# Optimization experiments

Measured on AMD Instinct MI355X. Metric: run time of the kernel, lower is better.

## Reference

```python
import jax, jax.numpy as jnp
import numpy as np

NPOINT = 1024
RADIUS = 0.5
NSAMPLE = 32
BN_EPS = 1e-5


def square_distance(src, dst):
    # src: (B,S,3), dst: (B,N,3) -> (B,S,N)
    return (jnp.sum(src ** 2, -1, keepdims=True)
            + jnp.swapaxes(jnp.sum(dst ** 2, -1, keepdims=True), -2, -1)
            - 2.0 * jnp.einsum('bsc,bnc->bsn', src, dst))


def farthest_point_sample(xyz, npoint):
    # xyz: (B,N,3) -> (B,npoint) int32. Deterministic start at index 0.
    B, N, _ = xyz.shape

    def step(carry, _):
        distance, farthest = carry
        centroid = jnp.take_along_axis(xyz, farthest[:, None, None], axis=1)  # (B,1,3)
        d = jnp.sum((xyz - centroid) ** 2, axis=-1)                           # (B,N)
        distance = jnp.minimum(distance, d)
        nxt = jnp.argmax(distance, axis=-1).astype(jnp.int32)
        return (distance, nxt), farthest

    init = (jnp.full((B, N), 1e10, dtype=xyz.dtype), jnp.zeros((B,), jnp.int32))
    _, cents = jax.lax.scan(step, init, None, length=npoint)  # (npoint,B)
    return cents.T


def ball_query(radius, nsample, xyz, new_xyz):
    # -> (B,S,nsample) int32 indices into N; empty slots padded with first hit.
    B, N, _ = xyz.shape
    dist = square_distance(new_xyz, xyz)                       # (B,S,N)
    base = jnp.arange(N, dtype=jnp.int32)[None, None, :]
    idx = jnp.where(dist <= radius ** 2, base, N)
    idx = jnp.sort(idx, axis=-1)[:, :, :nsample]
    first = idx[:, :, :1]
    return jnp.where(idx == N, first, idx)


def index_points(points, idx):
    # points: (B,N,C), idx: (B,...) -> (B,...,C)
    return jax.vmap(lambda p, i: p[i])(points, idx)


def _forward(xyz, features, params):
    # indices are data-dependent but non-differentiable selections
    xyz_c = jax.lax.stop_gradient(xyz)
    fps_idx = farthest_point_sample(xyz_c, NPOINT)             # (B,S)
    group_idx = ball_query(RADIUS, NSAMPLE, xyz_c, index_points(xyz_c, fps_idx))

    new_xyz = index_points(xyz, fps_idx)                       # (B,S,3)
    grouped_xyz = index_points(xyz, group_idx) - new_xyz[:, :, None, :]  # (B,S,K,3)
    grouped = jnp.concatenate([grouped_xyz, index_points(features, group_idx)], -1)  # (B,S,K,Cin)

    for (w, b, g, be) in params:
        # 1x1 Conv2d == per-point linear; BatchNorm2d in training mode:
        # stats over all but channel axis (here axes 0,1,2 of (B,S,K,C)).
        h = jnp.einsum('bskc,dc->bskd', grouped, w) + b
        mean = jnp.mean(h, axis=(0, 1, 2))
        var = jnp.var(h, axis=(0, 1, 2))
        h = (h - mean) * jax.lax.rsqrt(var + BN_EPS) * g + be
        grouped = jax.nn.gelu(h, approximate=False)

    new_features = jnp.max(grouped, axis=2)                    # (B,S,D)
    return new_xyz, new_features


def setup_inputs() -> dict:
    key = jax.random.key(0)
    ks = jax.random.split(key, 16)
    B, N, C = 16, 4096, 64
    inp = {
        'xyz': jax.random.normal(ks[0], (B, N, 3), jnp.float32),
        'features': jax.random.normal(ks[1], (B, N, C), jnp.float32),
    }
    chans = [67, 64, 64, 128]
    for i in range(3):
        cin, cout = chans[i], chans[i + 1]
        inp[f'w{i}'] = jax.random.normal(ks[2 + 4 * i], (cout, cin), jnp.float32) * (1.0 / np.sqrt(cin))
        inp[f'b{i}'] = jnp.zeros((cout,), jnp.float32)
        inp[f'g{i}'] = jnp.ones((cout,), jnp.float32)
        inp[f'be{i}'] = jnp.zeros((cout,), jnp.float32)
    return inp


def reference(xyz, features, w0, b0, g0, be0, w1, b1, g1, be1, w2, b2, g2, be2):
    params = [(w0, b0, g0, be0), (w1, b1, g1, be1), (w2, b2, g2, be2)]
    return _forward(xyz, features, params)
```

## Files before the change

### kernel.cpp

```cpp
#include <hip/hip_runtime.h>

typedef unsigned int uint;
typedef unsigned short ushort;

#define NB 16
#define NN 4096
#define NS 1024
#define NK 32
#define CIN0 67
#define NPTS (NB*NS*NK)
#define BN_EPS 1e-5f
#define INV_NPTS (1.0f/524288.0f)

#define W0T_OFF 0
#define W1T_OFF 4288
#define W2T_OFF 8384
#define WT_TOTAL 16576

#define FPS_T 256
#define PPT (NN / FPS_T)

__device__ __forceinline__ void amax_merge(float& bv, int& bi, float ov, int oi) {
  if (ov > bv || (ov == bv && oi < bi)) { bv = ov; bi = oi; }
}

#define DPP_AMAX_STEP(CTRL) do { \
    int _ov = __builtin_amdgcn_update_dpp(0, __float_as_int(bv), (CTRL), 0xF, 0xF, true); \
    int _oi = __builtin_amdgcn_update_dpp(0, bi,                 (CTRL), 0xF, 0xF, true); \
    amax_merge(bv, bi, __int_as_float(_ov), _oi); \
  } while (0)

__global__ __launch_bounds__(FPS_T) void fps_kernel(
    const float* __restrict__ xyz, float* __restrict__ centers,
    float* __restrict__ out_newxyz)
{
#pragma clang fp contract(off)
  __shared__ float4 sxyz[NN];
  __shared__ int sfar[NS];
  __shared__ __align__(16) uint2 sred[2][FPS_T/64];
  const int b = blockIdx.x;
  const int tid = threadIdx.x;
  const float* xb = xyz + (size_t)b * NN * 3;
  for (int i = tid; i < NN; i += FPS_T)
    sxyz[i] = make_float4(xb[i*3+0], xb[i*3+1], xb[i*3+2], 0.f);
  __syncthreads();
  float px[PPT], py[PPT], pz[PPT], dist[PPT];
  const int base = tid * PPT;
#pragma unroll
  for (int j = 0; j < PPT; ++j) {
    float4 P = sxyz[base+j];
    px[j] = P.x; py[j] = P.y; pz[j] = P.z;
    dist[j] = 1e10f;
  }
  float4 C0 = sxyz[0];
  float cx = C0.x, cy = C0.y, cz = C0.z;
  if (tid == 0) sfar[0] = 0;

  for (int it = 1; it < NS; ++it) {
#pragma unroll
    for (int j = 0; j < PPT; ++j) {
      float dx = px[j]-cx, dy = py[j]-cy, dz = pz[j]-cz;
      float d = (dx*dx + dy*dy) + dz*dz;
      float dd = dist[j];
      dist[j] = d < dd ? d : dd;
    }
    float v8[8]; int i8[8];
#pragma unroll
    for (int j = 0; j < 8; ++j) {
      bool t = dist[2*j+1] > dist[2*j];
      v8[j] = t ? dist[2*j+1] : dist[2*j];
      i8[j] = base + (t ? 2*j+1 : 2*j);
    }
    float v4[4]; int i4[4];
#pragma unroll
    for (int j = 0; j < 4; ++j) {
      bool t = v8[2*j+1] > v8[2*j];
      v4[j] = t ? v8[2*j+1] : v8[2*j];
      i4[j] = t ? i8[2*j+1] : i8[2*j];
    }
    float v2[2]; int i2[2];
#pragma unroll
    for (int j = 0; j < 2; ++j) {
      bool t = v4[2*j+1] > v4[2*j];
      v2[j] = t ? v4[2*j+1] : v4[2*j];
      i2[j] = t ? i4[2*j+1] : i4[2*j];
    }
    bool t0 = v2[1] > v2[0];
    float bv = t0 ? v2[1] : v2[0];
    int   bi = t0 ? i2[1] : i2[0];
    DPP_AMAX_STEP(0x121);
    DPP_AMAX_STEP(0x122);
    DPP_AMAX_STEP(0x124);
    DPP_AMAX_STEP(0x128);
    DPP_AMAX_STEP(0x142);
    DPP_AMAX_STEP(0x143);
    const int pb = it & 1;
    if ((tid & 63) == 63) sred[pb][tid>>6] = make_uint2(__float_as_uint(bv), (uint)bi);
    __syncthreads();
    uint4 ra = *((const uint4*)&sred[pb][0]);
    uint4 rb = *((const uint4*)&sred[pb][2]);
    float fv = __uint_as_float(ra.x); int fi = (int)ra.y;
    amax_merge(fv, fi, __uint_as_float(ra.z), (int)ra.w);
    amax_merge(fv, fi, __uint_as_float(rb.x), (int)rb.y);
    amax_merge(fv, fi, __uint_as_float(rb.z), (int)rb.w);
    float4 C = sxyz[fi];
    cx = C.x; cy = C.y; cz = C.z;
    if (tid == 0) sfar[it] = fi;
  }
  __syncthreads();
  for (int s = tid; s < NS; s += FPS_T) {
    int f = sfar[s];
    float4 C = sxyz[f];
    size_t o = ((size_t)b * NS + s) * 3;
    centers[o] = C.x; centers[o+1] = C.y; centers[o+2] = C.z;
    out_newxyz[o] = C.x; out_newxyz[o+1] = C.y; out_newxyz[o+2] = C.z;
  }
}

#define BPAD(i) ((i) + ((i)>>6))
__global__ __launch_bounds__(256,2) void ball_kernel(
    const float* __restrict__ xyz, const float* __restrict__ centers,
    int* __restrict__ group_idx)
{
#pragma clang fp contract(off)
  __shared__ float sx[4160], sy[4160], sz[4160], sq[4160];
  const int bid = blockIdx.x;
  const int b = bid >> 6;
  const int c0 = (bid & 63) << 4;
  const int tid = threadIdx.x;
  const int lane = tid & 63;
  const int wave = tid >> 6;
  const float* xb = xyz + (size_t)b * NN * 3;
  for (int i = tid; i < NN; i += 256) {
    float x = xb[i*3+0], y = xb[i*3+1], z = xb[i*3+2];
    int a = BPAD(i);
    sx[a] = x; sy[a] = y; sz[a] = z;
    sq[a] = (x*x + y*y) + z*z;
  }
  __syncthreads();
  const int a0 = lane * 65;
#pragma unroll 1
  for (int r = 0; r < 4; ++r) {
    const int s = c0 + wave*4 + r;
    const size_t co = ((size_t)b * NS + s) * 3;
    const float cx = centers[co], cy = centers[co+1], cz = centers[co+2];
    const float csq = (cx*cx + cy*cy) + cz*cz;
    unsigned long long mask = 0ull;
#pragma unroll 8
    for (int j = 0; j < 64; ++j) {
      const float dot = (cx*sx[a0+j] + cy*sy[a0+j]) + cz*sz[a0+j];
      const float dist = (csq + sq[a0+j]) - 2.0f*dot;
      mask |= ((unsigned long long)(dist <= 0.25f)) << j;
    }
    int cnt = __popcll(mask);
    int inc = cnt;
#pragma unroll
    for (int m = 1; m < 64; m <<= 1) {
      int o = __shfl_up(inc, m);
      if (lane >= m) inc += o;
    }
    const int pre = inc - cnt;
    const int total = __shfl(inc, 63);
    unsigned long long bal = __ballot(cnt > 0);
    int fl = __ffsll(bal) - 1;
    int myfirst = cnt ? (lane << 6) + __ffsll(mask) - 1 : 0;
    int firstG = __shfl(myfirst, fl);
    int* out = group_idx + ((size_t)b * NS + s) * NK;
    if (pre < NK && cnt) {
      int k = pre;
      unsigned long long m2 = mask;
      while (m2 && k < NK) {
        int j = __ffsll(m2) - 1;
        out[k++] = (lane << 6) + j;
        m2 &= m2 - 1;
      }
    }
    if (total < NK) {
      for (int q2 = total + lane; q2 < NK; q2 += 64) out[q2] = firstG;
    }
  }
}

__global__ __launch_bounds__(256) void prep_kernel(
    const float* __restrict__ w0, const float* __restrict__ w1,
    const float* __restrict__ w2, float* __restrict__ wT)
{
  int i = blockIdx.x*256 + threadIdx.x;
  if (i < 4288) {
    int c = i >> 6, d = i & 63;
    wT[i] = w0[d*CIN0 + c];
  } else if (i < 8384) {
    int j = i - 4288; int c = j >> 6, d = j & 63;
    wT[i] = w1[d*64 + c];
  } else if (i < WT_TOTAL) {
    int j = i - 8384; int c = j >> 7, d = j & 127;
    wT[i] = w2[d*64 + c];
  }
}

__device__ __forceinline__ float gelu_f(float x) {
  float z = fabsf(x) * 0.70710678118654752f;
  float t = __builtin_amdgcn_rcpf(fmaf(0.3275911f, z, 1.0f));
  float p = t * fmaf(t, fmaf(t, fmaf(t, fmaf(t, 1.061405429f, -1.453152027f),
                                     1.421413741f), -0.284496736f), 0.254829592f);
  float ex = __expf(-z*z);
  float er = fmaf(-p, ex, 1.0f);
  float se = __uint_as_float(__float_as_uint(er) | (__float_as_uint(x) & 0x80000000u));
  return 0.5f * x * (1.0f + se);
}
__device__ __forceinline__ float bf_lo(uint u) { return __uint_as_float(u << 16); }
__device__ __forceinline__ float bf_hi(uint u) { return __uint_as_float(u & 0xffff0000u); }
__device__ __forceinline__ uint bfpack(float a, float b) {
  uint ua = __float_as_uint(a), ub = __float_as_uint(b);
  ua = (ua + 0x7fffu + ((ua >> 16) & 1u)) >> 16;
  ub = (ub + 0x7fffu + ((ub >> 16) & 1u)) >> 16;
  return (ua & 0xffffu) | (ub << 16);
}

__device__ __forceinline__ void fmac64(float (&acc)[64], const float* wrow, float xc) {
  const float4* wp = (const float4*)wrow;
#pragma unroll
  for (int i = 0; i < 16; ++i) {
    float4 w = wp[i];
    acc[i*4+0] = fmaf(xc, w.x, acc[i*4+0]);
    acc[i*4+1] = fmaf(xc, w.y, acc[i*4+1]);
    acc[i*4+2] = fmaf(xc, w.z, acc[i*4+2]);
    acc[i*4+3] = fmaf(xc, w.w, acc[i*4+3]);
  }
}
__device__ __forceinline__ void fmac128(float (&acc)[128], const float* wrow, float xc) {
  const float4* wp = (const float4*)wrow;
#pragma unroll
  for (int i = 0; i < 32; ++i) {
    float4 w = wp[i];
    acc[i*4+0] = fmaf(xc, w.x, acc[i*4+0]);
    acc[i*4+1] = fmaf(xc, w.y, acc[i*4+1]);
    acc[i*4+2] = fmaf(xc, w.z, acc[i*4+2]);
    acc[i*4+3] = fmaf(xc, w.w, acc[i*4+3]);
  }
}

__device__ __forceinline__ void layer0(
    const float* __restrict__ xyz, const float* __restrict__ feat,
    const float* __restrict__ centers, const int* __restrict__ gidx,
    const float* wsh, const float* b0v, int p, float (&acc)[64])
{
  const int b = p >> 15;
  const int s = (p & 32767) >> 5;
  const int gi = gidx[p];
#pragma unroll
  for (int d = 0; d < 64; ++d) acc[d] = b0v[d];
  const float* cp = centers + ((size_t)(b*NS + s))*3;
  const float* pp = xyz + ((size_t)(b*NN) + gi)*3;
  const float4* fr = (const float4*)(feat + ((size_t)(b*NN) + gi)*64);
  float4 f = fr[0];
  fmac64(acc, wsh + 0*64, pp[0]-cp[0]);
  fmac64(acc, wsh + 1*64, pp[1]-cp[1]);
  fmac64(acc, wsh + 2*64, pp[2]-cp[2]);
#pragma unroll 1
  for (int q = 0; q < 16; ++q) {
    const int nq = (q < 15) ? q + 1 : 15;
    float4 fn = fr[nq];
    fmac64(acc, wsh + (3+q*4)*64, f.x);
    fmac64(acc, wsh + (4+q*4)*64, f.y);
    fmac64(acc, wsh + (5+q*4)*64, f.z);
    fmac64(acc, wsh + (6+q*4)*64, f.w);
    f = fn;
  }
}

__device__ __forceinline__ void block_colsum64(const float (&v)[64], float* sbuf,
    float* bsum, float* bssq, int cbase)
{
  const int tid = threadIdx.x;
#pragma unroll
  for (int cc = 0; cc < 4; ++cc) {
    __syncthreads();
#pragma unroll
    for (int j = 0; j < 16; ++j) sbuf[tid*17 + j] = v[cc*16 + j];
    __syncthreads();
    const int c = tid & 15, seg = tid >> 4;
    float s = 0.f, q = 0.f;
#pragma unroll
    for (int i = 0; i < 16; ++i) {
      float x = sbuf[(seg*16 + i)*17 + c];
      s += x; q += x*x;
    }
    __syncthreads();
    sbuf[tid*2] = s; sbuf[tid*2+1] = q;
    __syncthreads();
    if (tid < 16) {
      float ss = 0.f, qq = 0.f;
#pragma unroll
      for (int sg = 0; sg < 16; ++sg) {
        ss += sbuf[(sg*16 + tid)*2];
        qq += sbuf[(sg*16 + tid)*2 + 1];
      }
      bsum[cbase + cc*16 + tid] += ss;
      bssq[cbase + cc*16 + tid] += qq;
    }
  }
  __syncthreads();
}

__global__ __launch_bounds__(256,3) void p0_kernel(
    const float* __restrict__ xyz, const float* __restrict__ feat,
    const float* __restrict__ centers, const int* __restrict__ gidx,
    const float* __restrict__ wT, const float* __restrict__ b0,
    ushort* __restrict__ X, float* __restrict__ stat0)
{
  __shared__ float wsh[4288];
  __shared__ float sbuf[4352];
  __shared__ float bsum[64], bssq[64], b0s[64];
  const int tid = threadIdx.x;
  for (int i = tid; i < 1072; i += 256) ((float4*)wsh)[i] = ((const float4*)wT)[i];
  if (tid < 64) { bsum[tid] = 0.f; bssq[tid] = 0.f; b0s[tid] = b0[tid]; }
  __syncthreads();
  const int p = blockIdx.x*256 + tid;
  float acc[64];
  layer0(xyz, feat, centers, gidx, wsh, b0s, p, acc);
  uint4* xr = (uint4*)(X + (size_t)p*64);
#pragma unroll
  for (int q = 0; q < 8; ++q) {
    uint4 pk;
    pk.x = bfpack(acc[q*8+0], acc[q*8+1]);
    pk.y = bfpack(acc[q*8+2], acc[q*8+3]);
    pk.z = bfpack(acc[q*8+4], acc[q*8+5]);
    pk.w = bfpack(acc[q*8+6], acc[q*8+7]);
    xr[q] = pk;
  }
  block_colsum64(acc, sbuf, bsum, bssq, 0);
  if (tid < 64) {
    atomicAdd(&stat0[tid], bsum[tid]);
    atomicAdd(&stat0[64+tid], bssq[tid]);
  }
}

__global__ __launch_bounds__(256,3) void p1_kernel(
    ushort* X, const float* __restrict__ wT,
    const float* __restrict__ stat0, const float* __restrict__ g0,
    const float* __restrict__ be0, const float* __restrict__ b1,
    float* __restrict__ stat1)
{
  __shared__ float wsh[4096];
  __shared__ float sbuf[4352];
  __shared__ float bsum[64], bssq[64];
  __shared__ float sc[64], sh[64], b1s[64];
  const int tid = threadIdx.x;
  for (int i = tid; i < 1024; i += 256)
    ((float4*)wsh)[i] = ((const float4*)(wT + W1T_OFF))[i];
  if (tid < 64) {
    float m0 = stat0[tid]*INV_NPTS;
    float v0 = stat0[64+tid]*INV_NPTS - m0*m0;
    float s0 = (1.0f/sqrtf(v0 + BN_EPS)) * g0[tid];
    sc[tid] = s0; sh[tid] = be0[tid] - m0*s0;
    b1s[tid] = b1[tid];
    bsum[tid] = 0.f; bssq[tid] = 0.f;
  }
  __syncthreads();
  const int p = blockIdx.x*256 + tid;
  uint4* xr = (uint4*)(X + (size_t)p*64);
  float acc[64];
#pragma unroll
  for (int d = 0; d < 64; ++d) acc[d] = b1s[d];
  uint4 v = xr[0];
#pragma unroll 1
  for (int ch = 0; ch < 8; ++ch) {
    const int nc = (ch < 7) ? ch + 1 : 7;
    uint4 vn = xr[nc];
    const int c = ch*8;
    float x0 = gelu_f(fmaf(bf_lo(v.x), sc[c+0], sh[c+0]));
    float x1 = gelu_f(fmaf(bf_hi(v.x), sc[c+1], sh[c+1]));
    float x2 = gelu_f(fmaf(bf_lo(v.y), sc[c+2], sh[c+2]));
    float x3 = gelu_f(fmaf(bf_hi(v.y), sc[c+3], sh[c+3]));
    float x4 = gelu_f(fmaf(bf_lo(v.z), sc[c+4], sh[c+4]));
    float x5 = gelu_f(fmaf(bf_hi(v.z), sc[c+5], sh[c+5]));
    float x6 = gelu_f(fmaf(bf_lo(v.w), sc[c+6], sh[c+6]));
    float x7 = gelu_f(fmaf(bf_hi(v.w), sc[c+7], sh[c+7]));
    fmac64(acc, wsh + (c+0)*64, x0);
    fmac64(acc, wsh + (c+1)*64, x1);
    fmac64(acc, wsh + (c+2)*64, x2);
    fmac64(acc, wsh + (c+3)*64, x3);
    fmac64(acc, wsh + (c+4)*64, x4);
    fmac64(acc, wsh + (c+5)*64, x5);
    fmac64(acc, wsh + (c+6)*64, x6);
    fmac64(acc, wsh + (c+7)*64, x7);
    v = vn;
  }
#pragma unroll
  for (int q = 0; q < 8; ++q) {
    uint4 pk;
    pk.x = bfpack(acc[q*8+0], acc[q*8+1]);
    pk.y = bfpack(acc[q*8+2], acc[q*8+3]);
    pk.z = bfpack(acc[q*8+4], acc[q*8+5]);
    pk.w = bfpack(acc[q*8+6], acc[q*8+7]);
    xr[q] = pk;
  }
  block_colsum64(acc, sbuf, bsum, bssq, 0);
  if (tid < 64) {
    atomicAdd(&stat1[tid], bsum[tid]);
    atomicAdd(&stat1[64+tid], bssq[tid]);
  }
}

template<bool STORE_H2>
__global__ __launch_bounds__(256,2) void p2_kernel(
    ushort* X, ushort* __restrict__ H2, const float* __restrict__ wT,
    const float* __restrict__ stat1, const float* __restrict__ g1,
    const float* __restrict__ be1, const float* __restrict__ b2,
    float* __restrict__ stat2)
{
  __shared__ float wsh[8192];
  __shared__ float sbuf[4352];
  __shared__ float bsum[128], bssq[128];
  __shared__ float sc[64], sh[64], b2s[128];
  const int tid = threadIdx.x;
  for (int i = tid; i < 2048; i += 256)
    ((float4*)wsh)[i] = ((const float4*)(wT + W2T_OFF))[i];
  if (tid < 64) {
    float m1 = stat1[tid]*INV_NPTS;
    float v1 = stat1[64+tid]*INV_NPTS - m1*m1;
    float s1 = (1.0f/sqrtf(v1 + BN_EPS)) * g1[tid];
    sc[tid] = s1; sh[tid] = be1[tid] - m1*s1;
  }
  if (tid < 128) { b2s[tid] = b2[tid]; bsum[tid] = 0.f; bssq[tid] = 0.f; }
  __syncthreads();
  const int p = blockIdx.x*256 + tid;
  uint4* xr = (uint4*)(X + (size_t)p*64);
  float acc[128];
#pragma unroll
  for (int d = 0; d < 128; ++d) acc[d] = b2s[d];
  uint4 v = xr[0];
#pragma unroll 1
  for (int ch = 0; ch < 8; ++ch) {
    const int nc = (ch < 7) ? ch + 1 : 7;
    uint4 vn = xr[nc];
    const int c = ch*8;
    float x0 = gelu_f(fmaf(bf_lo(v.x), sc[c+0], sh[c+0]));
    float x1 = gelu_f(fmaf(bf_hi(v.x), sc[c+1], sh[c+1]));
    float x2 = gelu_f(fmaf(bf_lo(v.y), sc[c+2], sh[c+2]));
    float x3 = gelu_f(fmaf(bf_hi(v.y), sc[c+3], sh[c+3]));
    float x4 = gelu_f(fmaf(bf_lo(v.z), sc[c+4], sh[c+4]));
    float x5 = gelu_f(fmaf(bf_hi(v.z), sc[c+5], sh[c+5]));
    float x6 = gelu_f(fmaf(bf_lo(v.w), sc[c+6], sh[c+6]));
    float x7 = gelu_f(fmaf(bf_hi(v.w), sc[c+7], sh[c+7]));
    if (!STORE_H2) {
      uint4 pk;
      pk.x = bfpack(x0, x1); pk.y = bfpack(x2, x3);
      pk.z = bfpack(x4, x5); pk.w = bfpack(x6, x7);
      xr[ch] = pk;
    }
    fmac128(acc, wsh + (c+0)*128, x0);
    fmac128(acc, wsh + (c+1)*128, x1);
    fmac128(acc, wsh + (c+2)*128, x2);
    fmac128(acc, wsh + (c+3)*128, x3);
    fmac128(acc, wsh + (c+4)*128, x4);
    fmac128(acc, wsh + (c+5)*128, x5);
    fmac128(acc, wsh + (c+6)*128, x6);
    fmac128(acc, wsh + (c+7)*128, x7);
    v = vn;
  }
  if (STORE_H2) {
    uint4* hr = (uint4*)(H2 + (size_t)p*128);
#pragma unroll
    for (int q = 0; q < 16; ++q) {
      uint4 pk;
      pk.x = bfpack(acc[q*8+0], acc[q*8+1]);
      pk.y = bfpack(acc[q*8+2], acc[q*8+3]);
      pk.z = bfpack(acc[q*8+4], acc[q*8+5]);
      pk.w = bfpack(acc[q*8+6], acc[q*8+7]);
      hr[q] = pk;
    }
  }
#pragma unroll
  for (int half = 0; half < 2; ++half) {
    float tmp[64];
#pragma unroll
    for (int d = 0; d < 64; ++d) tmp[d] = acc[half*64 + d];
    block_colsum64(tmp, sbuf, bsum, bssq, half*64);
  }
  if (tid < 128) {
    atomicAdd(&stat2[tid], bsum[tid]);
    atomicAdd(&stat2[128+tid], bssq[tid]);
  }
}

__global__ __launch_bounds__(128) void fbig_kernel(
    const ushort* __restrict__ H2, const float* __restrict__ stat2,
    const float* __restrict__ g2, const float* __restrict__ be2,
    float* __restrict__ out_feat)
{
  const int d = threadIdx.x;
  const int bs = blockIdx.x;
  const float mean = stat2[d] * INV_NPTS;
  const float var  = stat2[128+d] * INV_NPTS - mean*mean;
  const float scale = (1.0f/sqrtf(var + BN_EPS)) * g2[d];
  const float shift = be2[d] - mean*scale;
  const ushort* rp = H2 + (size_t)bs*NK*128 + d;
  float m = -3.4e38f;
#pragma unroll 4
  for (int k = 0; k < NK; ++k) {
    float t = __uint_as_float(((uint)rp[k*128]) << 16);
    m = fmaxf(m, gelu_f(fmaf(t, scale, shift)));
  }
  out_feat[(size_t)bs*128 + d] = m;
}

__global__ __launch_bounds__(256,2) void fsmall_kernel(
    const ushort* __restrict__ X, const float* __restrict__ wT,
    const float* __restrict__ b2, const float* __restrict__ stat2,
    const float* __restrict__ g2, const float* __restrict__ be2,
    float* __restrict__ out_feat)
{
  __shared__ float wsh[8192];
  __shared__ float b2s[128], sc2[128], sh2[128];
  const int tid = threadIdx.x;
  for (int i = tid; i < 2048; i += 256)
    ((float4*)wsh)[i] = ((const float4*)(wT + W2T_OFF))[i];
  if (tid < 128) {
    b2s[tid] = b2[tid];
    float m2 = stat2[tid]*INV_NPTS;
    float v2 = stat2[128+tid]*INV_NPTS - m2*m2;
    float s2 = (1.0f/sqrtf(v2 + BN_EPS)) * g2[tid];
    sc2[tid] = s2; sh2[tid] = be2[tid] - m2*s2;
  }
  __syncthreads();
  const int p = blockIdx.x*256 + tid;
  const int bs = p >> 5;
  const uint4* xr = (const uint4*)(X + (size_t)p*64);
  float acc[128];
#pragma unroll
  for (int d = 0; d < 128; ++d) acc[d] = b2s[d];
  uint4 v = xr[0];
#pragma unroll 1
  for (int ch = 0; ch < 8; ++ch) {
    const int nc = (ch < 7) ? ch + 1 : 7;
    uint4 vn = xr[nc];
    const int c = ch*8;
    fmac128(acc, wsh + (c+0)*128, bf_lo(v.x));
    fmac128(acc, wsh + (c+1)*128, bf_hi(v.x));
    fmac128(acc, wsh + (c+2)*128, bf_lo(v.y));
    fmac128(acc, wsh + (c+3)*128, bf_hi(v.y));
    fmac128(acc, wsh + (c+4)*128, bf_lo(v.z));
    fmac128(acc, wsh + (c+5)*128, bf_hi(v.z));
    fmac128(acc, wsh + (c+6)*128, bf_lo(v.w));
    fmac128(acc, wsh + (c+7)*128, bf_hi(v.w));
    v = vn;
  }
#pragma unroll
  for (int d = 0; d < 128; ++d) {
    float y = gelu_f(fmaf(acc[d], sc2[d], sh2[d]));
#pragma unroll
    for (int m = 1; m < 32; m <<= 1) y = fmaxf(y, __shfl_xor(y, m));
    acc[d] = y;
  }
  if ((tid & 31) == 0) {
    float4* op = (float4*)(out_feat + (size_t)bs*128);
#pragma unroll
    for (int i = 0; i < 32; ++i)
      op[i] = make_float4(acc[i*4], acc[i*4+1], acc[i*4+2], acc[i*4+3]);
  }
}

__device__ __forceinline__ void chain_to_x2(
    const float* __restrict__ xyz, const float* __restrict__ feat,
    const float* __restrict__ centers, const int* __restrict__ gidx,
    const float* wsh, float* sbuf, const float* prm, int p, float (&x2)[64])
{
  float acc0[64];
  layer0(xyz, feat, centers, gidx, wsh, prm, p, acc0);
#pragma unroll
  for (int c = 0; c < 64; ++c) acc0[c] = gelu_f(fmaf(acc0[c], prm[64+c], prm[128+c]));
#pragma unroll
  for (int d = 0; d < 64; ++d) x2[d] = prm[192+d];
  float* xrow = sbuf + threadIdx.x*17;
#pragma unroll
  for (int cc = 0; cc < 4; ++cc) {
#pragma unroll
    for (int j = 0; j < 16; ++j) xrow[j] = acc0[cc*16 + j];
#pragma unroll 1
    for (int cj = 0; cj < 16; ++cj)
      fmac64(x2, wsh + W1T_OFF + (cc*16+cj)*64, xrow[cj]);
  }
#pragma unroll
  for (int c = 0; c < 64; ++c) x2[c] = gelu_f(fmaf(x2[c], prm[256+c], prm[320+c]));
}

__global__ __launch_bounds__(256,2) void s0_kernel(
    const float* __restrict__ xyz, const float* __restrict__ feat,
    const float* __restrict__ centers, const int* __restrict__ gidx,
    const float* __restrict__ wT, const float* __restrict__ b0,
    float* __restrict__ stat0)
{
  __shared__ float wsh[4288];
  __shared__ float sbuf[4352];
  __shared__ float bsum[64], bssq[64], b0s[64];
  const int tid = threadIdx.x;
  for (int i = tid; i < 1072; i += 256) ((float4*)wsh)[i] = ((const float4*)wT)[i];
  if (tid < 64) { bsum[tid] = 0.f; bssq[tid] = 0.f; b0s[tid] = b0[tid]; }
  __syncthreads();
  const int p = blockIdx.x*256 + tid;
  float acc[64];
  layer0(xyz, feat, centers, gidx, wsh, b0s, p, acc);
  block_colsum64(acc, sbuf, bsum, bssq, 0);
  if (tid < 64) {
    atomicAdd(&stat0[tid], bsum[tid]);
    atomicAdd(&stat0[64+tid], bssq[tid]);
  }
}

__global__ __launch_bounds__(256,2) void s1_kernel(
    const float* __restrict__ xyz, const float* __restrict__ feat,
    const float* __restrict__ centers, const int* __restrict__ gidx,
    const float* __restrict__ wT, const float* __restrict__ stat0,
    const float* __restrict__ g0, const float* __restrict__ be0,
    const float* __restrict__ b0, const float* __restrict__ b1,
    float* __restrict__ stat1)
{
  __shared__ float wsh[8384];
  __shared__ float sbuf[4352];
  __shared__ float bsum[64], bssq[64];
  __shared__ float prm[256];
  const int tid = threadIdx.x;
  for (int i = tid; i < 2096; i += 256) ((float4*)wsh)[i] = ((const float4*)wT)[i];
  if (tid < 64) {
    float m0 = stat0[tid]*INV_NPTS;
    float v0 = stat0[64+tid]*INV_NPTS - m0*m0;
    float sc0 = (1.0f/sqrtf(v0 + BN_EPS)) * g0[tid];
    prm[tid] = b0[tid]; prm[64+tid] = sc0; prm[128+tid] = be0[tid] - m0*sc0;
// ... 123 lines not shown
  float x2[64];
  chain_to_x2(xyz, feat, centers, gidx, wsh, sbuf, prm, p, x2);
  __syncthreads();
  for (int i = tid; i < 2048; i += 256)
    ((float4*)wsh)[i] = ((const float4*)(wT + W2T_OFF))[i];
  __syncthreads();
  float* xrow = sbuf + tid*17;
#pragma unroll 1
  for (int half = 0; half < 2; ++half) {
    float a2[64];
#pragma unroll
    for (int d = 0; d < 64; ++d) a2[d] = prm[384 + half*64 + d];
#pragma unroll
    for (int cc = 0; cc < 4; ++cc) {
#pragma unroll
      for (int j = 0; j < 16; ++j) xrow[j] = x2[cc*16 + j];
#pragma unroll 1
      for (int cj = 0; cj < 16; ++cj)
        fmac64(a2, wsh + (cc*16+cj)*128 + half*64, xrow[cj]);
    }
#pragma unroll
    for (int d = 0; d < 64; ++d) {
      float y = gelu_f(fmaf(a2[d], prm[512 + half*64 + d], prm[640 + half*64 + d]));
#pragma unroll
      for (int m = 1; m < 32; m <<= 1) y = fmaxf(y, __shfl_xor(y, m));
      a2[d] = y;
    }
    if ((tid & 31) == 0) {
      float4* op = (float4*)(out_feat + ((size_t)(b*NS + s))*128 + half*64);
#pragma unroll
      for (int i = 0; i < 16; ++i)
        op[i] = make_float4(a2[i*4], a2[i*4+1], a2[i*4+2], a2[i*4+3]);
    }
  }
}

extern "C" void kernel_launch(void* const* d_in, const int* in_sizes, int n_in,
                              void* d_out, int out_size, void* d_ws, size_t ws_size,
                              hipStream_t stream) {
  (void)in_sizes; (void)n_in; (void)out_size;
  const float* xyz      = (const float*)d_in[0];
  const float* features = (const float*)d_in[1];
  const float* w0  = (const float*)d_in[2];
  const float* b0  = (const float*)d_in[3];
  const float* g0  = (const float*)d_in[4];
  const float* be0 = (const float*)d_in[5];
  const float* w1  = (const float*)d_in[6];
  const float* b1  = (const float*)d_in[7];
  const float* g1  = (const float*)d_in[8];
  const float* be1 = (const float*)d_in[9];
  const float* w2  = (const float*)d_in[10];
  const float* b2  = (const float*)d_in[11];
  const float* g2  = (const float*)d_in[12];
  const float* be2 = (const float*)d_in[13];

  float* out = (float*)d_out;
  float* out_newxyz = out;
  float* out_feat   = out + NB*NS*3;

  char* ws = (char*)d_ws;
  size_t off = 0;
  float* centers   = (float*)(ws + off); off += (size_t)NB*NS*3*4;
  int*   group_idx = (int*)(ws + off);   off += (size_t)NPTS*4;
  float* stats     = (float*)(ws + off); off += 512*4;
  off = (off + 255) & ~(size_t)255;
  float* wT        = (float*)(ws + off); off += (size_t)WT_TOTAL*4;
  off = (off + 255) & ~(size_t)255;
  const size_t base_end = off;
  const size_t X_bytes  = (size_t)NPTS*64*2;
  const size_t H2_bytes = (size_t)NPTS*128*2;
  ushort* X  = (ushort*)(ws + base_end);
  ushort* H2 = (ushort*)(ws + base_end + X_bytes);

  const bool tier_big   = ws_size >= base_end + X_bytes + H2_bytes;
  const bool tier_small = !tier_big && ws_size >= base_end + X_bytes;
  if (ws_size < base_end) return;

  float* stat0 = stats;
  float* stat1 = stats + 128;
  float* stat2 = stats + 256;

  (void)hipMemsetAsync(stats, 0, 2048, stream);
  prep_kernel<<<65, 256, 0, stream>>>(w0, w1, w2, wT);
  fps_kernel<<<NB, FPS_T, 0, stream>>>(xyz, centers, out_newxyz);
  ball_kernel<<<NB*64, 256, 0, stream>>>(xyz, centers, group_idx);

  if (tier_big || tier_small) {
    p0_kernel<<<NPTS/256, 256, 0, stream>>>(xyz, features, centers, group_idx,
                                            wT, b0, X, stat0);
    p1_kernel<<<NPTS/256, 256, 0, stream>>>(X, wT, stat0, g0, be0, b1, stat1);
    if (tier_big) {
      p2_kernel<true><<<NPTS/256, 256, 0, stream>>>(X, H2, wT, stat1, g1, be1, b2, stat2);
      fbig_kernel<<<NB*NS, 128, 0, stream>>>(H2, stat2, g2, be2, out_feat);
    } else {
      p2_kernel<false><<<NPTS/256, 256, 0, stream>>>(X, H2, wT, stat1, g1, be1, b2, stat2);
      fsmall_kernel<<<NPTS/256, 256, 0, stream>>>(X, wT, b2, stat2, g2, be2, out_feat);
    }
  } else {
    s0_kernel<<<NPTS/256, 256, 0, stream>>>(xyz, features, centers, group_idx, wT, b0, stat0);
    s1_kernel<<<NPTS/256, 256, 0, stream>>>(xyz, features, centers, group_idx, wT,
                                            stat0, g0, be0, b0, b1, stat1);
    s2_kernel<<<NPTS/256, 256, 0, stream>>>(xyz, features, centers, group_idx, wT,
                                            stat0, g0, be0, b0, b1, stat1, g1, be1, b2, stat2);
    fin_kernel<<<NPTS/256, 256, 0, stream>>>(xyz, features, centers, group_idx, wT,
                                             stat0, g0, be0, b0, b1, stat1, g1, be1, b2,
                                             stat2, g2, be2, out_feat);
  }
}
```

Measured before the change: 1.642 ms.

## Process two batches per FPS block and pack argmax into 64-bit keys

The farthest-point-sampling kernel now handles two batch elements per workgroup, interleaving their independent reductions so one barrier per iteration serves both. The argmax is packed into a single 64-bit key (distance bits, inverted index), so the ties-to-lowest-index compare becomes one integer comparison. The winning wave also writes its center coordinates to LDS, which removes the dependent LDS lookup after the block merge. This halves the grid to 8 blocks and doubles register and LDS use per block, trading parallelism across CUs for better latency hiding on the serial, barrier-bound loop.

```diff
diff --git a/kernel.cpp b/kernel.cpp
--- a/kernel.cpp
+++ b/kernel.cpp
@@ -2,6 +2,7 @@
 
 typedef unsigned int uint;
 typedef unsigned short ushort;
+typedef unsigned long long ull;
 
 #define NB 16
 #define NN 4096
@@ -17,103 +18,148 @@
 #define W2T_OFF 8384
 #define WT_TOTAL 16576
 
-#define FPS_T 256
-#define PPT (NN / FPS_T)
-
-__device__ __forceinline__ void amax_merge(float& bv, int& bi, float ov, int oi) {
-  if (ov > bv || (ov == bv && oi < bi)) { bv = ov; bi = oi; }
-}
-
-#define DPP_AMAX_STEP(CTRL) do { \
-    int _ov = __builtin_amdgcn_update_dpp(0, __float_as_int(bv), (CTRL), 0xF, 0xF, true); \
-    int _oi = __builtin_amdgcn_update_dpp(0, bi,                 (CTRL), 0xF, 0xF, true); \
-    amax_merge(bv, bi, __int_as_float(_ov), _oi); \
+#define PPT 16
+
+#define KMAX_STEP(K, CTRL) do { \
+    uint _lo = (uint)(K), _hi = (uint)((K) >> 32); \
+    uint _nlo = (uint)__builtin_amdgcn_update_dpp(0, (int)_lo, (CTRL), 0xF, 0xF, true); \
+    uint _nhi = (uint)__builtin_amdgcn_update_dpp(0, (int)_hi, (CTRL), 0xF, 0xF, true); \
+    ull _nk = ((ull)_nhi << 32) | _nlo; \
+    if (_nk > (K)) (K) = _nk; \
   } while (0)
 
-__global__ __launch_bounds__(FPS_T) void fps_kernel(
+__device__ __forceinline__ ull fps_wave_reduce(
+    float (&px)[PPT], float (&py)[PPT], float (&pz)[PPT], float (&dist)[PPT],
+    float cx, float cy, float cz, int base)
+{
+#pragma clang fp contract(off)
+#pragma unroll
+  for (int j = 0; j < PPT; ++j) {
+    float dx = px[j]-cx, dy = py[j]-cy, dz = pz[j]-cz;
+    float d = (dx*dx + dy*dy) + dz*dz;
+    float dd = dist[j];
+    dist[j] = d < dd ? d : dd;
+  }
+  float v8[8]; int i8[8];
+#pragma unroll
+  for (int j = 0; j < 8; ++j) {
+    bool t = dist[2*j+1] > dist[2*j];
+    v8[j] = t ? dist[2*j+1] : dist[2*j];
+    i8[j] = base + (t ? 2*j+1 : 2*j);
+  }
+  float v4[4]; int i4[4];
+#pragma unroll
+  for (int j = 0; j < 4; ++j) {
+    bool t = v8[2*j+1] > v8[2*j];
+    v4[j] = t ? v8[2*j+1] : v8[2*j];
+    i4[j] = t ? i8[2*j+1] : i8[2*j];
+  }
+  float v2[2]; int i2[2];
+#pragma unroll
+  for (int j = 0; j < 2; ++j) {
+    bool t = v4[2*j+1] > v4[2*j];
+    v2[j] = t ? v4[2*j+1] : v4[2*j];
+    i2[j] = t ? i4[2*j+1] : i4[2*j];
+  }
+  bool t0 = v2[1] > v2[0];
+  float bv = t0 ? v2[1] : v2[0];
+  int   bi = t0 ? i2[1] : i2[0];
+  ull key = ((ull)__float_as_uint(bv) << 32) | (uint)(~bi);
+  KMAX_STEP(key, 0x121);
+  KMAX_STEP(key, 0x122);
+  KMAX_STEP(key, 0x124);
+  KMAX_STEP(key, 0x128);
+  KMAX_STEP(key, 0x142);
+  KMAX_STEP(key, 0x143);
+  return key;
+}
+
+__device__ __forceinline__ void fps_block_merge(
+    const uint2* sk, const float4* sc,
+    float& cx, float& cy, float& cz, int& fi)
+{
+  uint4 e01 = *(const uint4*)&sk[0];
+  uint4 e23 = *(const uint4*)&sk[2];
+  ull k0 = ((ull)e01.y << 32) | e01.x;
+  ull k1 = ((ull)e01.w << 32) | e01.z;
+  ull k2 = ((ull)e23.y << 32) | e23.x;
+  ull k3 = ((ull)e23.w << 32) | e23.z;
+  float4 c0 = sc[0], c1 = sc[1], c2 = sc[2], c3 = sc[3];
+  ull b = k0; float4 C = c0;
+  if (k1 > b) { b = k1; C = c1; }
+  if (k2 > b) { b = k2; C = c2; }
+  if (k3 > b) { b = k3; C = c3; }
+  cx = C.x; cy = C.y; cz = C.z;
+  fi = (int)(~(uint)b);
+}
+
+__global__ __launch_bounds__(256) void fps_kernel(
     const float* __restrict__ xyz, float* __restrict__ centers,
     float* __restrict__ out_newxyz)
 {
 #pragma clang fp contract(off)
-  __shared__ float4 sxyz[NN];
-  __shared__ int sfar[NS];
-  __shared__ __align__(16) uint2 sred[2][FPS_T/64];
-  const int b = blockIdx.x;
-  const int tid = threadIdx.x;
-  const float* xb = xyz + (size_t)b * NN * 3;
-  for (int i = tid; i < NN; i += FPS_T)
-    sxyz[i] = make_float4(xb[i*3+0], xb[i*3+1], xb[i*3+2], 0.f);
-  __syncthreads();
-  float px[PPT], py[PPT], pz[PPT], dist[PPT];
+  __shared__ float4 sA[NN], sB[NN];
+  __shared__ int sfarA[NS], sfarB[NS];
+  __shared__ __align__(16) uint2  skA[2][4], skB[2][4];
+  __shared__ __align__(16) float4 scA[2][4], scB[2][4];
+  const int bA = blockIdx.x * 2;
+  const int bB = bA + 1;
+  const int tid = threadIdx.x;
+  const int lane = tid & 63;
+  const int wv = tid >> 6;
+  const float* xbA = xyz + (size_t)bA * NN * 3;
+  const float* xbB = xyz + (size_t)bB * NN * 3;
+  for (int i = tid; i < NN; i += 256) {
+    sA[i] = make_float4(xbA[i*3+0], xbA[i*3+1], xbA[i*3+2], 0.f);
+    sB[i] = make_float4(xbB[i*3+0], xbB[i*3+1], xbB[i*3+2], 0.f);
+  }
+  __syncthreads();
+  float pxA[PPT], pyA[PPT], pzA[PPT], dA[PPT];
+  float pxB[PPT], pyB[PPT], pzB[PPT], dB[PPT];
   const int base = tid * PPT;
 #pragma unroll
   for (int j = 0; j < PPT; ++j) {
-    float4 P = sxyz[base+j];
-    px[j] = P.x; py[j] = P.y; pz[j] = P.z;
-    dist[j] = 1e10f;
-  }
-  float4 C0 = sxyz[0];
-  float cx = C0.x, cy = C0.y, cz = C0.z;
-  if (tid == 0) sfar[0] = 0;
+    float4 PA = sA[base+j]; float4 PB = sB[base+j];
+    pxA[j] = PA.x; pyA[j] = PA.y; pzA[j] = PA.z; dA[j] = 1e10f;
+    pxB[j] = PB.x; pyB[j] = PB.y; pzB[j] = PB.z; dB[j] = 1e10f;
+  }
+  float4 C0A = sA[0], C0B = sB[0];
+  float cxA = C0A.x, cyA = C0A.y, czA = C0A.z;
+  float cxB = C0B.x, cyB = C0B.y, czB = C0B.z;
+  if (tid == 0) { sfarA[0] = 0; sfarB[0] = 0; }
 
   for (int it = 1; it < NS; ++it) {
-#pragma unroll
-    for (int j = 0; j < PPT; ++j) {
-      float dx = px[j]-cx, dy = py[j]-cy, dz = pz[j]-cz;
-      float d = (dx*dx + dy*dy) + dz*dz;
-      float dd = dist[j];
-      dist[j] = d < dd ? d : dd;
-    }
-    float v8[8]; int i8[8];
-#pragma unroll
-    for (int j = 0; j < 8; ++j) {
-      bool t = dist[2*j+1] > dist[2*j];
-      v8[j] = t ? dist[2*j+1] : dist[2*j];
-      i8[j] = base + (t ? 2*j+1 : 2*j);
-    }
-    float v4[4]; int i4[4];
-#pragma unroll
-    for (int j = 0; j < 4; ++j) {
-      bool t = v8[2*j+1] > v8[2*j];
-      v4[j] = t ? v8[2*j+1] : v8[2*j];
-      i4[j] = t ? i8[2*j+1] : i8[2*j];
-    }
-    float v2[2]; int i2[2];
-#pragma unroll
-    for (int j = 0; j < 2; ++j) {
-      bool t = v4[2*j+1] > v4[2*j];
-      v2[j] = t ? v4[2*j+1] : v4[2*j];
-      i2[j] = t ? i4[2*j+1] : i4[2*j];
-    }
-    bool t0 = v2[1] > v2[0];
-    float bv = t0 ? v2[1] : v2[0];
-    int   bi = t0 ? i2[1] : i2[0];
-    DPP_AMAX_STEP(0x121);
-    DPP_AMAX_STEP(0x122);
-    DPP_AMAX_STEP(0x124);
-    DPP_AMAX_STEP(0x128);
-    DPP_AMAX_STEP(0x142);
-    DPP_AMAX_STEP(0x143);
+    ull kA = fps_wave_reduce(pxA, pyA, pzA, dA, cxA, cyA, czA, base);
+    ull kB = fps_wave_reduce(pxB, pyB, pzB, dB, cxB, cyB, czB, base);
     const int pb = it & 1;
-    if ((tid & 63) == 63) sred[pb][tid>>6] = make_uint2(__float_as_uint(bv), (uint)bi);
+    if (lane == 63) {
+      int iA = (int)(~(uint)kA);
+      int iB = (int)(~(uint)kB);
+      float4 CA = sA[iA];
+      float4 CB = sB[iB];
+      skA[pb][wv] = make_uint2((uint)kA, (uint)(kA >> 32));
+      skB[pb][wv] = make_uint2((uint)kB, (uint)(kB >> 32));
+      scA[pb][wv] = CA;
+      scB[pb][wv] = CB;
+    }
     __syncthreads();
-    uint4 ra = *((const uint4*)&sred[pb][0]);
-    uint4 rb = *((const uint4*)&sred[pb][2]);
-    float fv = __uint_as_float(ra.x); int fi = (int)ra.y;
-    amax_merge(fv, fi, __uint_as_float(ra.z), (int)ra.w);
-    amax_merge(fv, fi, __uint_as_float(rb.x), (int)rb.y);
-    amax_merge(fv, fi, __uint_as_float(rb.z), (int)rb.w);
-    float4 C = sxyz[fi];
-    cx = C.x; cy = C.y; cz = C.z;
-    if (tid == 0) sfar[it] = fi;
-  }
-  __syncthreads();
-  for (int s = tid; s < NS; s += FPS_T) {
-    int f = sfar[s];
-    float4 C = sxyz[f];
-    size_t o = ((size_t)b * NS + s) * 3;
-    centers[o] = C.x; centers[o+1] = C.y; centers[o+2] = C.z;
-    out_newxyz[o] = C.x; out_newxyz[o+1] = C.y; out_newxyz[o+2] = C.z;
+    int fiA, fiB;
+    fps_block_merge(skA[pb], scA[pb], cxA, cyA, czA, fiA);
+    fps_block_merge(skB[pb], scB[pb], cxB, cyB, czB, fiB);
+    if (tid == 0) { sfarA[it] = fiA; sfarB[it] = fiB; }
+  }
+  __syncthreads();
+  for (int s = tid; s < NS; s += 256) {
+    int fA = sfarA[s];
+    float4 CA = sA[fA];
+    size_t oA = ((size_t)bA * NS + s) * 3;
+    centers[oA] = CA.x; centers[oA+1] = CA.y; centers[oA+2] = CA.z;
+    out_newxyz[oA] = CA.x; out_newxyz[oA+1] = CA.y; out_newxyz[oA+2] = CA.z;
+    int fB = sfarB[s];
+    float4 CB = sB[fB];
+    size_t oB = ((size_t)bB * NS + s) * 3;
+    centers[oB] = CB.x; centers[oB+1] = CB.y; centers[oB+2] = CB.z;
+    out_newxyz[oB] = CB.x; out_newxyz[oB+1] = CB.y; out_newxyz[oB+2] = CB.z;
   }
 }
 
@@ -834,7 +880,7 @@
 
   (void)hipMemsetAsync(stats, 0, 2048, stream);
   prep_kernel<<<65, 256, 0, stream>>>(w0, w1, w2, wT);
-  fps_kernel<<<NB, FPS_T, 0, stream>>>(xyz, centers, out_newxyz);
+  fps_kernel<<<NB/2, 256, 0, stream>>>(xyz, centers, out_newxyz);
   ball_kernel<<<NB*64, 256, 0, stream>>>(xyz, centers, group_idx);
 
   if (tier_big || tier_small) {
```

Result: slower. 2.136 ms (+30.1%).

## Run FPS in a single wavefront and read MLP weights directly from global memory

Applied to the files above, without the earlier changes.

The farthest-point-sampling kernel drops from 256 threads to one 64-lane wavefront per batch, with 64 points per lane. This removes the per-iteration __syncthreads and shared-memory cross-wave reduction. The argmax is done with a packed 64-bit key (distance bits plus inverted index) reduced via DPP and read back with readlane. Separately, the p0/p1/p2/fsmall kernels no longer stage weights in LDS and read them from global memory instead, relying on uniform cached loads. The risks are heavy register pressure in FPS (256 floats per lane), less parallelism per batch, and slower weight access in the MLP kernels if scalar or L1 caching does not serve them well.

```diff
diff --git a/kernel.cpp b/kernel.cpp
--- a/kernel.cpp
+++ b/kernel.cpp
@@ -2,6 +2,7 @@
 
 typedef unsigned int uint;
 typedef unsigned short ushort;
+typedef unsigned long long ull;
 
 #define NB 16
 #define NN 4096
@@ -17,35 +18,31 @@
 #define W2T_OFF 8384
 #define WT_TOTAL 16576
 
-#define FPS_T 256
-#define PPT (NN / FPS_T)
-
-__device__ __forceinline__ void amax_merge(float& bv, int& bi, float ov, int oi) {
-  if (ov > bv || (ov == bv && oi < bi)) { bv = ov; bi = oi; }
-}
-
-#define DPP_AMAX_STEP(CTRL) do { \
-    int _ov = __builtin_amdgcn_update_dpp(0, __float_as_int(bv), (CTRL), 0xF, 0xF, true); \
-    int _oi = __builtin_amdgcn_update_dpp(0, bi,                 (CTRL), 0xF, 0xF, true); \
-    amax_merge(bv, bi, __int_as_float(_ov), _oi); \
+#define PPT 64
+
+#define KMAX_STEP(K, CTRL) do { \
+    uint _lo = (uint)(K), _hi = (uint)((K) >> 32); \
+    uint _nlo = (uint)__builtin_amdgcn_update_dpp(0, (int)_lo, (CTRL), 0xF, 0xF, true); \
+    uint _nhi = (uint)__builtin_amdgcn_update_dpp(0, (int)_hi, (CTRL), 0xF, 0xF, true); \
+    ull _nk = ((ull)_nhi << 32) | _nlo; \
+    if (_nk > (K)) (K) = _nk; \
   } while (0)
 
-__global__ __launch_bounds__(FPS_T) void fps_kernel(
+__global__ __launch_bounds__(64) void fps_kernel(
     const float* __restrict__ xyz, float* __restrict__ centers,
     float* __restrict__ out_newxyz)
 {
 #pragma clang fp contract(off)
   __shared__ float4 sxyz[NN];
   __shared__ int sfar[NS];
-  __shared__ __align__(16) uint2 sred[2][FPS_T/64];
   const int b = blockIdx.x;
-  const int tid = threadIdx.x;
+  const int lane = threadIdx.x;
   const float* xb = xyz + (size_t)b * NN * 3;
-  for (int i = tid; i < NN; i += FPS_T)
+  for (int i = lane; i < NN; i += 64)
     sxyz[i] = make_float4(xb[i*3+0], xb[i*3+1], xb[i*3+2], 0.f);
   __syncthreads();
   float px[PPT], py[PPT], pz[PPT], dist[PPT];
-  const int base = tid * PPT;
+  const int base = lane * PPT;
 #pragma unroll
   for (int j = 0; j < PPT; ++j) {
     float4 P = sxyz[base+j];
@@ -54,7 +51,7 @@
   }
   float4 C0 = sxyz[0];
   float cx = C0.x, cy = C0.y, cz = C0.z;
-  if (tid == 0) sfar[0] = 0;
+  if (lane == 0) sfar[0] = 0;
 
   for (int it = 1; it < NS; ++it) {
 #pragma unroll
@@ -64,51 +61,37 @@
       float dd = dist[j];
       dist[j] = d < dd ? d : dd;
     }
-    float v8[8]; int i8[8];
-#pragma unroll
-    for (int j = 0; j < 8; ++j) {
+    float v[32]; int id[32];
+#pragma unroll
+    for (int j = 0; j < 32; ++j) {
       bool t = dist[2*j+1] > dist[2*j];
-      v8[j] = t ? dist[2*j+1] : dist[2*j];
-      i8[j] = base + (t ? 2*j+1 : 2*j);
-    }
-    float v4[4]; int i4[4];
-#pragma unroll
-    for (int j = 0; j < 4; ++j) {
-      bool t = v8[2*j+1] > v8[2*j];
-      v4[j] = t ? v8[2*j+1] : v8[2*j];
-      i4[j] = t ? i8[2*j+1] : i8[2*j];
-    }
-    float v2[2]; int i2[2];
-#pragma unroll
-    for (int j = 0; j < 2; ++j) {
-      bool t = v4[2*j+1] > v4[2*j];
-      v2[j] = t ? v4[2*j+1] : v4[2*j];
-      i2[j] = t ? i4[2*j+1] : i4[2*j];
-    }
-    bool t0 = v2[1] > v2[0];
-    float bv = t0 ? v2[1] : v2[0];
-    int   bi = t0 ? i2[1] : i2[0];
-    DPP_AMAX_STEP(0x121);
-    DPP_AMAX_STEP(0x122);
-    DPP_AMAX_STEP(0x124);
-    DPP_AMAX_STEP(0x128);
-    DPP_AMAX_STEP(0x142);
-    DPP_AMAX_STEP(0x143);
-    const int pb = it & 1;
-    if ((tid & 63) == 63) sred[pb][tid>>6] = make_uint2(__float_as_uint(bv), (uint)bi);
-    __syncthreads();
-    uint4 ra = *((const uint4*)&sred[pb][0]);
-    uint4 rb = *((const uint4*)&sred[pb][2]);
-    float fv = __uint_as_float(ra.x); int fi = (int)ra.y;
-    amax_merge(fv, fi, __uint_as_float(ra.z), (int)ra.w);
-    amax_merge(fv, fi, __uint_as_float(rb.x), (int)rb.y);
-    amax_merge(fv, fi, __uint_as_float(rb.z), (int)rb.w);
+      v[j] = t ? dist[2*j+1] : dist[2*j];
+      id[j] = base + (t ? 2*j+1 : 2*j);
+    }
+#pragma unroll
+    for (int w = 16; w >= 1; w >>= 1) {
+#pragma unroll
+      for (int j = 0; j < w; ++j) {
+        bool t = v[2*j+1] > v[2*j];
+        v[j] = t ? v[2*j+1] : v[2*j];
+        id[j] = t ? id[2*j+1] : id[2*j];
+      }
+    }
+    ull key = ((ull)__float_as_uint(v[0]) << 32) | (uint)(~id[0]);
+    KMAX_STEP(key, 0x121);
+    KMAX_STEP(key, 0x122);
+    KMAX_STEP(key, 0x124);
+    KMAX_STEP(key, 0x128);
+    KMAX_STEP(key, 0x142);
+    KMAX_STEP(key, 0x143);
+    int klo = __builtin_amdgcn_readlane((int)(uint)key, 63);
+    int fi = (int)(~(uint)klo);
+    if (lane == 0) sfar[it] = fi;
     float4 C = sxyz[fi];
     cx = C.x; cy = C.y; cz = C.z;
-    if (tid == 0) sfar[it] = fi;
-  }
-  __syncthreads();
-  for (int s = tid; s < NS; s += FPS_T) {
+  }
+  __syncthreads();
+  for (int s = lane; s < NS; s += 64) {
     int f = sfar[s];
     float4 C = sxyz[f];
     size_t o = ((size_t)b * NS + s) * 3;
@@ -243,7 +226,7 @@
 __device__ __forceinline__ void layer0(
     const float* __restrict__ xyz, const float* __restrict__ feat,
     const float* __restrict__ centers, const int* __restrict__ gidx,
-    const float* wsh, const float* b0v, int p, float (&acc)[64])
+    const float* wptr, const float* b0v, int p, float (&acc)[64])
 {
   const int b = p >> 15;
   const int s = (p & 32767) >> 5;
@@ -254,17 +237,17 @@
   const float* pp = xyz + ((size_t)(b*NN) + gi)*3;
   const float4* fr = (const float4*)(feat + ((size_t)(b*NN) + gi)*64);
   float4 f = fr[0];
-  fmac64(acc, wsh + 0*64, pp[0]-cp[0]);
-  fmac64(acc, wsh + 1*64, pp[1]-cp[1]);
-  fmac64(acc, wsh + 2*64, pp[2]-cp[2]);
+  fmac64(acc, wptr + 0*64, pp[0]-cp[0]);
+  fmac64(acc, wptr + 1*64, pp[1]-cp[1]);
+  fmac64(acc, wptr + 2*64, pp[2]-cp[2]);
 #pragma unroll 1
   for (int q = 0; q < 16; ++q) {
     const int nq = (q < 15) ? q + 1 : 15;
     float4 fn = fr[nq];
-    fmac64(acc, wsh + (3+q*4)*64, f.x);
-    fmac64(acc, wsh + (4+q*4)*64, f.y);
-    fmac64(acc, wsh + (5+q*4)*64, f.z);
-    fmac64(acc, wsh + (6+q*4)*64, f.w);
+    fmac64(acc, wptr + (3+q*4)*64, f.x);
+    fmac64(acc, wptr + (4+q*4)*64, f.y);
+    fmac64(acc, wptr + (5+q*4)*64, f.z);
+    fmac64(acc, wptr + (6+q*4)*64, f.w);
     f = fn;
   }
 }
@@ -309,16 +292,14 @@
     const float* __restrict__ wT, const float* __restrict__ b0,
     ushort* __restrict__ X, float* __restrict__ stat0)
 {
-  __shared__ float wsh[4288];
   __shared__ float sbuf[4352];
   __shared__ float bsum[64], bssq[64], b0s[64];
   const int tid = threadIdx.x;
-  for (int i = tid; i < 1072; i += 256) ((float4*)wsh)[i] = ((const float4*)wT)[i];
   if (tid < 64) { bsum[tid] = 0.f; bssq[tid] = 0.f; b0s[tid] = b0[tid]; }
   __syncthreads();
   const int p = blockIdx.x*256 + tid;
   float acc[64];
-  layer0(xyz, feat, centers, gidx, wsh, b0s, p, acc);
+  layer0(xyz, feat, centers, gidx, wT + W0T_OFF, b0s, p, acc);
   uint4* xr = (uint4*)(X + (size_t)p*64);
 #pragma unroll
   for (int q = 0; q < 8; ++q) {
@@ -342,13 +323,11 @@
     const float* __restrict__ be0, const float* __restrict__ b1,
     float* __restrict__ stat1)
 {
-  __shared__ float wsh[4096];
   __shared__ float sbuf[4352];
   __shared__ float bsum[64], bssq[64];
   __shared__ float sc[64], sh[64], b1s[64];
-  const int tid = threadIdx.x;
-  for (int i = tid; i < 1024; i += 256)
-    ((float4*)wsh)[i] = ((const float4*)(wT + W1T_OFF))[i];
+  const float* __restrict__ w1g = wT + W1T_OFF;
+  const int tid = threadIdx.x;
   if (tid < 64) {
     float m0 = stat0[tid]*INV_NPTS;
     float v0 = stat0[64+tid]*INV_NPTS - m0*m0;
@@ -377,14 +356,14 @@
     float x5 = gelu_f(fmaf(bf_hi(v.z), sc[c+5], sh[c+5]));
     float x6 = gelu_f(fmaf(bf_lo(v.w), sc[c+6], sh[c+6]));
     float x7 = gelu_f(fmaf(bf_hi(v.w), sc[c+7], sh[c+7]));
-    fmac64(acc, wsh + (c+0)*64, x0);
-    fmac64(acc, wsh + (c+1)*64, x1);
-    fmac64(acc, wsh + (c+2)*64, x2);
-    fmac64(acc, wsh + (c+3)*64, x3);
-    fmac64(acc, wsh + (c+4)*64, x4);
-    fmac64(acc, wsh + (c+5)*64, x5);
-    fmac64(acc, wsh + (c+6)*64, x6);
-    fmac64(acc, wsh + (c+7)*64, x7);
+    fmac64(acc, w1g + (c+0)*64, x0);
+    fmac64(acc, w1g + (c+1)*64, x1);
+    fmac64(acc, w1g + (c+2)*64, x2);
+    fmac64(acc, w1g + (c+3)*64, x3);
+    fmac64(acc, w1g + (c+4)*64, x4);
+    fmac64(acc, w1g + (c+5)*64, x5);
+    fmac64(acc, w1g + (c+6)*64, x6);
+    fmac64(acc, w1g + (c+7)*64, x7);
     v = vn;
   }
 #pragma unroll
@@ -410,13 +389,11 @@
     const float* __restrict__ be1, const float* __restrict__ b2,
     float* __restrict__ stat2)
 {
-  __shared__ float wsh[8192];
   __shared__ float sbuf[4352];
   __shared__ float bsum[128], bssq[128];
   __shared__ float sc[64], sh[64], b2s[128];
-  const int tid = threadIdx.x;
-  for (int i = tid; i < 2048; i += 256)
-    ((float4*)wsh)[i] = ((const float4*)(wT + W2T_OFF))[i];
+  const float* __restrict__ w2g = wT + W2T_OFF;
+  const int tid = threadIdx.x;
   if (tid < 64) {
     float m1 = stat1[tid]*INV_NPTS;
     float v1 = stat1[64+tid]*INV_NPTS - m1*m1;
@@ -450,14 +427,14 @@
       pk.z = bfpack(x4, x5); pk.w = bfpack(x6, x7);
       xr[ch] = pk;
     }
-    fmac128(acc, wsh + (c+0)*128, x0);
-    fmac128(acc, wsh + (c+1)*128, x1);
-    fmac128(acc, wsh + (c+2)*128, x2);
-    fmac128(acc, wsh + (c+3)*128, x3);
-    fmac128(acc, wsh + (c+4)*128, x4);
-    fmac128(acc, wsh + (c+5)*128, x5);
-    fmac128(acc, wsh + (c+6)*128, x6);
-    fmac128(acc, wsh + (c+7)*128, x7);
+    fmac128(acc, w2g + (c+0)*128, x0);
+    fmac128(acc, w2g + (c+1)*128, x1);
+    fmac128(acc, w2g + (c+2)*128, x2);
+    fmac128(acc, w2g + (c+3)*128, x3);
+    fmac128(acc, w2g + (c+4)*128, x4);
+    fmac128(acc, w2g + (c+5)*128, x5);
+    fmac128(acc, w2g + (c+6)*128, x6);
+    fmac128(acc, w2g + (c+7)*128, x7);
     v = vn;
   }
   if (STORE_H2) {
@@ -512,11 +489,9 @@
     const float* __restrict__ g2, const float* __restrict__ be2,
     float* __restrict__ out_feat)
 {
-  __shared__ float wsh[8192];
   __shared__ float b2s[128], sc2[128], sh2[128];
-  const int tid = threadIdx.x;
-  for (int i = tid; i < 2048; i += 256)
-    ((float4*)wsh)[i] = ((const float4*)(wT + W2T_OFF))[i];
+  const float* __restrict__ w2g = wT + W2T_OFF;
+  const int tid = threadIdx.x;
   if (tid < 128) {
     b2s[tid] = b2[tid];
     float m2 = stat2[tid]*INV_NPTS;
@@ -537,14 +512,14 @@
     const int nc = (ch < 7) ? ch + 1 : 7;
     uint4 vn = xr[nc];
     const int c = ch*8;
-    fmac128(acc, wsh + (c+0)*128, bf_lo(v.x));
-    fmac128(acc, wsh + (c+1)*128, bf_hi(v.x));
-    fmac128(acc, wsh + (c+2)*128, bf_lo(v.y));
-    fmac128(acc, wsh + (c+3)*128, bf_hi(v.y));
-    fmac128(acc, wsh + (c+4)*128, bf_lo(v.z));
-    fmac128(acc, wsh + (c+5)*128, bf_hi(v.z));
-    fmac128(acc, wsh + (c+6)*128, bf_lo(v.w));
-    fmac128(acc, wsh + (c+7)*128, bf_hi(v.w));
+    fmac128(acc, w2g + (c+0)*128, bf_lo(v.x));
+    fmac128(acc, w2g + (c+1)*128, bf_hi(v.x));
+    fmac128(acc, w2g + (c+2)*128, bf_lo(v.y));
+    fmac128(acc, w2g + (c+3)*128, bf_hi(v.y));
+    fmac128(acc, w2g + (c+4)*128, bf_lo(v.z));
+    fmac128(acc, w2g + (c+5)*128, bf_hi(v.z));
+    fmac128(acc, w2g + (c+6)*128, bf_lo(v.w));
+    fmac128(acc, w2g + (c+7)*128, bf_hi(v.w));
     v = vn;
   }
 #pragma unroll
@@ -834,7 +809,7 @@
 
   (void)hipMemsetAsync(stats, 0, 2048, stream);
   prep_kernel<<<65, 256, 0, stream>>>(w0, w1, w2, wT);
-  fps_kernel<<<NB, FPS_T, 0, stream>>>(xyz, centers, out_newxyz);
+  fps_kernel<<<NB, 64, 0, stream>>>(xyz, centers, out_newxyz);
   ball_kernel<<<NB*64, 256, 0, stream>>>(xyz, centers, group_idx);
 
   if (tier_big || tier_small) {
```

Result: slower. 5.370 ms (+226.9%).
